# Kernel optimization log

Measured on AMD Instinct MI355X. Metric: run time of the kernel, lower is better.

## Reference

```python
import jax, jax.numpy as jnp
import numpy as np

NUM_HEADS = 16
D_MODEL = 1024
HEAD_DIM = D_MODEL // NUM_HEADS
EPS = 1e-6


def setup_inputs() -> dict:
    key = jax.random.key(0)
    ks = jax.random.split(key, 9)
    B, S, D = 4, 8192, D_MODEL
    scale = 1.0 / np.sqrt(D)  # variance_scaling(1.0, fan_in, normal) approx
    inputs_q = jax.random.normal(ks[0], (B, S, D), dtype=jnp.float32)
    Wq = jax.random.normal(ks[1], (D, D), dtype=jnp.float32) * scale
    Wk = jax.random.normal(ks[2], (D, D), dtype=jnp.float32) * scale
    Wv = jax.random.normal(ks[3], (D, D), dtype=jnp.float32) * scale
    Wo = jax.random.normal(ks[4], (D, D), dtype=jnp.float32) * scale
    bq = jnp.zeros((D,), jnp.float32)
    bk = jnp.zeros((D,), jnp.float32)
    bv = jnp.zeros((D,), jnp.float32)
    bo = jnp.zeros((D,), jnp.float32)
    return {"inputs_q": inputs_q, "Wq": Wq, "bq": bq, "Wk": Wk, "bk": bk,
            "Wv": Wv, "bv": bv, "Wo": Wo, "bo": bo}


def _feature_map(x):
    return jax.nn.elu(x) + 1.0


def reference(inputs_q, Wq, bq, Wk, bk, Wv, bv, Wo, bo):
    B, S, D = inputs_q.shape
    H, Dh = NUM_HEADS, HEAD_DIM
    # QKV projections (self-attention: k,v inputs default to q input)
    q = (inputs_q @ Wq + bq).reshape(B, S, H, Dh)
    k = (inputs_q @ Wk + bk).reshape(B, S, H, Dh)
    v = (inputs_q @ Wv + bv).reshape(B, S, H, Dh)
    q = _feature_map(q)
    k = _feature_map(k)
    # KV outer-product accumulation: [B, H, Dh, Dh]
    kv = jnp.einsum('bkhd,bkhm->bhdm', k, v)
    out = jnp.einsum('bqhd,bhdm->bqhm', q, kv)
    # normalizer: q . sum_k(k)
    normalizer = jnp.einsum('bqhd,bkhd->bqh', q, k)
    normalizer = jnp.maximum(normalizer, EPS)
    out = out / normalizer[..., None]
    out = out.reshape(B, S, D)
    return out @ Wo + bo
```

## Files before the change

### kernel.cpp

```cpp
#include <hip/hip_runtime.h>
#include <cstdint>
#include <cstddef>

#define D_MODEL 1024
#define SEQ 8192

typedef __bf16  bf16x8 __attribute__((ext_vector_type(8)));
typedef short   short8 __attribute__((ext_vector_type(8)));
typedef float   f32x4  __attribute__((ext_vector_type(4)));
typedef unsigned short ushort_t;

__device__ __forceinline__ ushort_t f2bf(float f) {
  uint32_t u = __builtin_bit_cast(uint32_t, f);
  u += 0x7FFFu + ((u >> 16) & 1u);
  return (ushort_t)(u >> 16);
}
__device__ __forceinline__ void gll16(const void* g, void* l) {
  __builtin_amdgcn_global_load_lds(
      (const __attribute__((address_space(1))) void*)g,
      (__attribute__((address_space(3))) void*)l, 16, 0, 0);
}
__device__ __forceinline__ void stage_half(const ushort_t* g, char* l0) {
  gll16(g, l0);
  gll16(g + 65536, l0 + 8192);
}

__global__ void k_convert_x(const float* __restrict__ x, ushort_t* __restrict__ xb, int n) {
  int i = (blockIdx.x * 256 + threadIdx.x) * 8;
  if (i >= n) return;
  float4 v0 = *(const float4*)(x + i);
  float4 v1 = *(const float4*)(x + i + 4);
  ushort_t o[8] = { f2bf(v0.x), f2bf(v0.y), f2bf(v0.z), f2bf(v0.w),
                    f2bf(v1.x), f2bf(v1.y), f2bf(v1.z), f2bf(v1.w) };
  *(short8*)(xb + i) = *(const short8*)o;
}

__global__ void k_transpose_w(const float* W0, const float* W1, const float* W2, const float* W3,
                              ushort_t* Tqkv, ushort_t* To) {
  const float* src; ushort_t* dst;
  switch (blockIdx.z) {
    case 0: src = W0; dst = Tqkv; break;
    case 1: src = W1; dst = Tqkv + (size_t)1024 * 1024; break;
    case 2: src = W2; dst = Tqkv + (size_t)2048 * 1024; break;
    default: src = W3; dst = To; break;
  }
  __shared__ float tile[64][65];
  int tx = threadIdx.x;
  int c = tx & 63, r0 = tx >> 6;
  int bx = blockIdx.x * 64, by = blockIdx.y * 64;
  #pragma unroll
  for (int i = 0; i < 16; i++) {
    int r = i * 4 + r0;
    tile[r][c] = src[(size_t)(by + r) * D_MODEL + bx + c];
  }
  __syncthreads();
  #pragma unroll
  for (int i = 0; i < 16; i++) {
    int r = i * 4 + r0;
    dst[(size_t)(bx + r) * D_MODEL + by + c] = f2bf(tile[c][r]);
  }
}

template<int MODE, int NY>
__global__ __launch_bounds__(512, 2) void k_gemm(const ushort_t* __restrict__ A,
                                                 const ushort_t* __restrict__ Bt,
                                                 const float* __restrict__ b0,
                                                 const float* __restrict__ b1,
                                                 const float* __restrict__ b2,
                                                 ushort_t* __restrict__ o0,
                                                 ushort_t* __restrict__ o1,
                                                 ushort_t* __restrict__ o2,
                                                 float* __restrict__ outf) {
  __shared__ __align__(16) char smem[131072];

  const int nwg = gridDim.x;
  const int bid0 = blockIdx.x;
  const int bid = (bid0 & 7) * (nwg >> 3) + (bid0 >> 3);
  const int xb = bid / NY, yb = bid % NY;
  const int m0 = xb * 256, n0 = yb * 256;

  const int tid = threadIdx.x;
  const int ln = tid & 63;
  const int w  = tid >> 6;
  const int wb = __builtin_amdgcn_readfirstlane(w);
  const int wm = wb >> 2, wn = wb & 3;

  const int srow = wb * 8 + (ln >> 3);
  const int schk = ((ln & 7) ^ ((ln >> 3) & 7)) * 8;
  const ushort_t* gA = A  + (size_t)(m0 + srow) * D_MODEL + schk;
  const ushort_t* gB = Bt + (size_t)(n0 + srow) * D_MODEL + schk;

#define STAGE_A(BUF, H, T) stage_half(gA + (size_t)(T) * 64 + (size_t)(H) * 131072, (BUF) + (H) * 16384 + wb * 1024)
#define STAGE_B(BUF, H, T) stage_half(gB + (size_t)(T) * 64 + (size_t)(H) * 131072, (BUF) + 32768 + (H) * 16384 + wb * 1024)

  char* cur = smem;
  char* nxt = smem + 65536;
  STAGE_B(cur, 0, 0); STAGE_B(cur, 1, 0); STAGE_A(cur, 0, 0); STAGE_A(cur, 1, 0);
  STAGE_B(nxt, 0, 1); STAGE_B(nxt, 1, 1); STAGE_A(nxt, 0, 1);
  asm volatile("s_waitcnt vmcnt(6)" ::: "memory");
  __builtin_amdgcn_s_barrier();

  f32x4 acc[8][4];
  #pragma unroll
  for (int i = 0; i < 8; i++)
    #pragma unroll
    for (int j = 0; j < 4; j++) acc[i][j] = (f32x4){0.f, 0.f, 0.f, 0.f};
  bf16x8 fa[4][2], fb0[2][2], fb1[2][2];

  const int ar  = ln & 15;
  const int cw0 = (((ln >> 4)    ) ^ (ln & 7)) << 4;
  const int cw1 = (((ln >> 4) + 4) ^ (ln & 7)) << 4;
  const int arow = wm * 128 + ar;
  const int brow = wn * 64 + ar;

#define LDA(MH) { _Pragma("unroll") for (int mi = 0; mi < 4; ++mi) { \
    const char* p_ = cur + ((arow + (MH) * 64 + mi * 16) << 7); \
    fa[mi][0] = *(const bf16x8*)(p_ + cw0); fa[mi][1] = *(const bf16x8*)(p_ + cw1); } }
#define LDB(FB, NH) { _Pragma("unroll") for (int nj = 0; nj < 2; ++nj) { \
    const char* p_ = cur + 32768 + ((brow + (NH) * 32 + nj * 16) << 7); \
    FB[nj][0] = *(const bf16x8*)(p_ + cw0); FB[nj][1] = *(const bf16x8*)(p_ + cw1); } }
#define QUAD(MH, NH, FB) { _Pragma("unroll") for (int mi = 0; mi < 4; ++mi) \
    _Pragma("unroll") for (int nj = 0; nj < 2; ++nj) { \
      acc[(MH)*4+mi][(NH)*2+nj] = __builtin_amdgcn_mfma_f32_16x16x32_bf16(fa[mi][0], FB[nj][0], acc[(MH)*4+mi][(NH)*2+nj], 0, 0, 0); \
      acc[(MH)*4+mi][(NH)*2+nj] = __builtin_amdgcn_mfma_f32_16x16x32_bf16(fa[mi][1], FB[nj][1], acc[(MH)*4+mi][(NH)*2+nj], 0, 0, 0); } }
#define PHASE_SYNC { __builtin_amdgcn_s_barrier(); \
                     asm volatile("s_waitcnt lgkmcnt(0)" ::: "memory"); \
                     __builtin_amdgcn_sched_barrier(0); }

  #pragma unroll 2
  for (int kt = 0; kt < 16; ++kt) {
    const bool st1 = (kt + 1 < 16);
    const bool st2 = (kt + 2 < 16);
    LDA(0); LDB(fb0, 0);
    if (st1) STAGE_A(nxt, 1, kt + 1);
    PHASE_SYNC;
    __builtin_amdgcn_s_setprio(1); QUAD(0, 0, fb0); __builtin_amdgcn_s_setprio(0);
    __builtin_amdgcn_s_barrier();
    LDB(fb1, 1);
    PHASE_SYNC;
    __builtin_amdgcn_s_setprio(1); QUAD(0, 1, fb1); __builtin_amdgcn_s_setprio(0);
    __builtin_amdgcn_s_barrier();
    LDA(1);
    if (st2) STAGE_B(cur, 0, kt + 2);
    PHASE_SYNC;
    __builtin_amdgcn_s_setprio(1); QUAD(1, 1, fb1); __builtin_amdgcn_s_setprio(0);
    __builtin_amdgcn_s_barrier();
    if (st2) { STAGE_B(cur, 1, kt + 2); STAGE_A(cur, 0, kt + 2); }
    __builtin_amdgcn_s_barrier();
    __builtin_amdgcn_s_setprio(1); QUAD(1, 0, fb0); __builtin_amdgcn_s_setprio(0);
    if (kt < 14)       asm volatile("s_waitcnt vmcnt(6)" ::: "memory");
    else if (kt == 14) asm volatile("s_waitcnt vmcnt(0)" ::: "memory");
    __builtin_amdgcn_s_barrier();
    char* t_ = cur; cur = nxt; nxt = t_;
  }
#undef STAGE_A
#undef STAGE_B
#undef LDA
#undef LDB
#undef QUAD
#undef PHASE_SYNC

  const int colb = ln & 15, rowb = (ln >> 4) * 4;

  if constexpr (MODE == 0) {
    const int region = yb >> 2;
    const int nl0 = (yb & 3) * 256;
    const float* bias = region == 0 ? b0 : (region == 1 ? b1 : b2);
    ushort_t* gout    = region == 0 ? o0 : (region == 1 ? o1 : o2);
    const bool act = region < 2;
    ushort_t* Cs = (ushort_t*)smem;
    #pragma unroll
    for (int j = 0; j < 4; ++j) {
      const int col = wn * 64 + j * 16 + colb;
      const float bv_ = bias[nl0 + col];
      #pragma unroll
      for (int i = 0; i < 8; ++i) {
        const int rb_ = wm * 128 + i * 16 + rowb;
        #pragma unroll
        for (int r = 0; r < 4; ++r) {
          float v = acc[i][j][r] + bv_;
          if (act) v = (v > 0.f) ? v + 1.f : __expf(v);
          const int row = rb_ + r;
          const int ch = col >> 3;
          Cs[row * 256 + ((ch ^ (row & 31)) << 3) + (col & 7)] = f2bf(v);
        }
      }
    }
    __syncthreads();
    #pragma unroll
    for (int c = 0; c < 16; ++c) {
      const int idx = c * 512 + tid;
      const int row = idx >> 5, ch = idx & 31;
      short8 t = *(const short8*)&Cs[row * 256 + ((ch ^ (row & 31)) << 3)];
      *(short8*)&gout[(size_t)(m0 + row) * D_MODEL + nl0 + ch * 8] = t;
    }
  } else {
    float* Cf = (float*)smem;
    #pragma unroll
    for (int h = 0; h < 2; ++h) {
      if (h) __syncthreads();
      if (wm == h) {
        #pragma unroll
        for (int j = 0; j < 4; ++j) {
          const int col = wn * 64 + j * 16 + colb;
          const float bv_ = b0[n0 + col];
          #pragma unroll
          for (int i = 0; i < 8; ++i) {
            const int rl = i * 16 + rowb;
            #pragma unroll
            for (int r = 0; r < 4; ++r) {
              const int row = rl + r;
              const int ch = col >> 2;
              Cf[row * 256 + ((ch ^ (row & 7)) << 2) + (col & 3)] = acc[i][j][r] + bv_;
            }
          }
        }
      }
      __syncthreads();
      #pragma unroll
      for (int c = 0; c < 16; ++c) {
        const int idx = c * 512 + tid;
        const int row = idx >> 6, ch = idx & 63;
        float4 t = *(const float4*)&Cf[row * 256 + ((ch ^ (row & 7)) << 2)];
        *(float4*)&outf[(size_t)(m0 + h * 128 + row) * D_MODEL + n0 + ch * 4] = t;
      }
    }
  }
}

__global__ __launch_bounds__(256) void k_kv_partial(const ushort_t* __restrict__ kmat,
                                                    const ushort_t* __restrict__ vmat,
                                                    float* __restrict__ part) {
  __shared__ __align__(16) ushort_t sbuf[4][2][2][512];
  const int tid = threadIdx.x, ln = tid & 63, w = tid >> 6;
  const int wb = __builtin_amdgcn_readfirstlane(w);
  const int bh = blockIdx.y, chunk = blockIdx.x;
  const int b = bh >> 4, h = bh & 15;
  const size_t cbase = ((size_t)b * SEQ + chunk * 1024 + w * 256) * D_MODEL + h * 64;
  const ushort_t* gk = kmat + cbase + (size_t)(ln >> 3) * D_MODEL + (ln & 7) * 8;
  const ushort_t* gv = vmat + cbase + (size_t)(ln >> 3) * D_MODEL + (ln & 7) * 8;

  float acc[8][8];
  float ksum[8];
  #pragma unroll
  for (int i = 0; i < 8; i++) { ksum[i] = 0.f;
    #pragma unroll
    for (int j = 0; j < 8; j++) acc[i][j] = 0.f; }

  const int r8 = (ln >> 3) * 8, c8 = (ln & 7) * 8;
  gll16(gk, &sbuf[wb][0][0][0]);
  gll16(gv, &sbuf[wb][0][1][0]);
  gk += 8 * D_MODEL; gv += 8 * D_MODEL;

  for (int bt = 0; bt < 32; bt++) {
    const int p = bt & 1;
    if (bt < 31) {
      gll16(gk, &sbuf[wb][p ^ 1][0][0]);
      gll16(gv, &sbuf[wb][p ^ 1][1][0]);
      gk += 8 * D_MODEL; gv += 8 * D_MODEL;
      __builtin_amdgcn_s_waitcnt(0x0F72);
    } else {
      __builtin_amdgcn_s_waitcnt(0x0F70);
    }
    #pragma unroll
    for (int s = 0; s < 8; s++) {
      short8 kk = *(const short8*)&sbuf[wb][p][0][s * 64 + r8];
      short8 vv = *(const short8*)&sbuf[wb][p][1][s * 64 + c8];
      float ka[8], va[8];
      #pragma unroll
      for (int i = 0; i < 8; i++) {
        ka[i] = __builtin_bit_cast(float, (uint32_t)(ushort_t)kk[i] << 16);
        va[i] = __builtin_bit_cast(float, (uint32_t)(ushort_t)vv[i] << 16);
      }
      #pragma unroll
      for (int i = 0; i < 8; i++) {
        ksum[i] += ka[i];
        #pragma unroll
        for (int j = 0; j < 8; j++) acc[i][j] += ka[i] * va[j];
      }
    }
  }
  float* p0 = part + ((size_t)bh * 32 + chunk * 4 + w) * 4160;
  #pragma unroll
  for (int i = 0; i < 8; i++)
    #pragma unroll
    for (int j = 0; j < 8; j++) p0[(r8 + i) * 64 + c8 + j] = acc[i][j];
  if ((ln & 7) == 0) {
    #pragma unroll
    for (int i = 0; i < 8; i++) p0[4096 + r8 + i] = ksum[i];
  }
}

__global__ void k_kv_reduce(const float* __restrict__ part, ushort_t* __restrict__ kvt) {
  const int bh = blockIdx.x, tid = threadIdx.x;
  const float* p0 = part + (size_t)bh * 32 * 4160;
  for (int idx = tid; idx < 4160; idx += 256) {
    float s = 0.f;
    #pragma unroll 4
    for (int c = 0; c < 32; c++) s += p0[(size_t)c * 4160 + idx];
    ushort_t bf = f2bf(s);
    if (idx < 4096) { int d = idx >> 6, m = idx & 63; kvt[(size_t)bh * 4160 + m * 64 + d] = bf; }
    else            { kvt[(size_t)bh * 4160 + 4096 + (idx - 4096)] = bf; }
  }
}

__global__ __launch_bounds__(256) void k_attn(const ushort_t* __restrict__ qmat,
                                              const ushort_t* __restrict__ kvt,
                                              ushort_t* __restrict__ attn) {
  __shared__ __align__(16) ushort_t kvs[65 * 80];
  __shared__ __align__(16) ushort_t qs[4][64 * 80];
  const int tid = threadIdx.x, ln = tid & 63, w = tid >> 6;
  const int bh = blockIdx.y, b = bh >> 4, h = bh & 15;

  for (int idx = tid; idx < 4160; idx += 256) {
    int m = idx >> 6, d = idx & 63;
    kvs[m * 80 + d] = kvt[(size_t)bh * 4160 + idx];
  }
  const size_t s0 = (size_t)b * SEQ + blockIdx.x * 256 + w * 64;
  #pragma unroll
  for (int c = 0; c < 8; c++) {
    int f = c * 64 + ln;
    int row = f >> 3, dg = (f & 7) * 8;
    short8 t = *(const short8*)&qmat[(s0 + row) * D_MODEL + h * 64 + dg];
    *(short8*)&qs[w][row * 80 + dg] = t;
  }
  __syncthreads();

  const int ar = ln & 15, aq = (ln >> 4) * 8;
  f32x4 acc[4][4], nacc[4];
  #pragma unroll
  for (int i = 0; i < 4; i++) { nacc[i] = (f32x4){0.f, 0.f, 0.f, 0.f};
    #pragma unroll
    for (int j = 0; j < 4; j++) acc[i][j] = (f32x4){0.f, 0.f, 0.f, 0.f}; }

  #pragma unroll
  for (int kk = 0; kk < 2; kk++) {
    const int ko = kk * 32 + aq;
    bf16x8 a[4], bb[4], bn;
    #pragma unroll
    for (int i = 0; i < 4; i++) a[i] = *(const bf16x8*)&qs[w][(i * 16 + ar) * 80 + ko];
    #pragma unroll
    for (int j = 0; j < 4; j++) bb[j] = *(const bf16x8*)&kvs[(j * 16 + ar) * 80 + ko];
    bn = *(const bf16x8*)&kvs[64 * 80 + ko];
    #pragma unroll
    for (int i = 0; i < 4; i++) {
      #pragma unroll
      for (int j = 0; j < 4; j++)
        acc[i][j] = __builtin_amdgcn_mfma_f32_16x16x32_bf16(a[i], bb[j], acc[i][j], 0, 0, 0);
      nacc[i] = __builtin_amdgcn_mfma_f32_16x16x32_bf16(a[i], bn, nacc[i], 0, 0, 0);
    }
  }

  const int colb = ln & 15, rowb = (ln >> 4) * 4;
  #pragma unroll
  for (int i = 0; i < 4; i++) {
    #pragma unroll
    for (int r = 0; r < 4; r++) {
      const int row = i * 16 + rowb + r;
      float nm = fmaxf(nacc[i][r], 1e-6f);
      float inv = 1.0f / nm;
      const size_t grow = s0 + row;
      #pragma unroll
      for (int j = 0; j < 4; j++) {
        float v = acc[i][j][r] * inv;
        attn[grow * D_MODEL + h * 64 + j * 16 + colb] = f2bf(v);
      }
    }
  }
}

extern "C" void kernel_launch(void* const* d_in, const int* in_sizes, int n_in,
                              void* d_out, int out_size, void* d_ws, size_t ws_size,
                              hipStream_t stream) {
  const float* x  = (const float*)d_in[0];
  const float* Wq = (const float*)d_in[1];
  const float* bq = (const float*)d_in[2];
  const float* Wk = (const float*)d_in[3];
  const float* bk = (const float*)d_in[4];
  const float* Wv = (const float*)d_in[5];
  const float* bv = (const float*)d_in[6];
  const float* Wo = (const float*)d_in[7];
  const float* bo = (const float*)d_in[8];
  float* out = (float*)d_out;

  const int M = in_sizes[0] / D_MODEL;
  const int B = M / SEQ;
  const int BH = B * 16;

  char* ws = (char*)d_ws;
  size_t off = 0;
  auto alloc = [&](size_t bytes) { char* p = ws + off; off += (bytes + 255) & ~(size_t)255; return p; };
  const size_t mb = (size_t)M * D_MODEL * 2;
  ushort_t* xb    = (ushort_t*)alloc(mb);
  ushort_t* qb    = (ushort_t*)alloc(mb);
  ushort_t* kb    = (ushort_t*)alloc(mb);
  ushort_t* vb    = (ushort_t*)alloc(mb);
  ushort_t* attnb = (ushort_t*)alloc(mb);
  ushort_t* wqkvt = (ushort_t*)alloc((size_t)3 * D_MODEL * D_MODEL * 2);
  ushort_t* wot   = (ushort_t*)alloc((size_t)D_MODEL * D_MODEL * 2);
  ushort_t* kvt   = (ushort_t*)alloc((size_t)BH * 4160 * 2);
  float*    part  = (float*)   alloc((size_t)BH * 32 * 4160 * 4);
  (void)ws_size; (void)n_in; (void)out_size;

  const int n = M * D_MODEL;
  k_convert_x<<<n / (256 * 8), 256, 0, stream>>>(x, xb, n);
  k_transpose_w<<<dim3(16, 16, 4), 256, 0, stream>>>(Wq, Wk, Wv, Wo, wqkvt, wot);

  k_gemm<0, 12><<<(M / 256) * 12, 512, 0, stream>>>(xb, wqkvt, bq, bk, bv, qb, kb, vb, nullptr);

  k_kv_partial<<<dim3(8, BH), 256, 0, stream>>>(kb, vb, part);
  k_kv_reduce<<<BH, 256, 0, stream>>>(part, kvt);
  k_attn<<<dim3(SEQ / 256, BH), 256, 0, stream>>>(qb, kvt, attnb);

  k_gemm<2, 4><<<(M / 256) * 4, 512, 0, stream>>>(attnb, wot, bo, nullptr, nullptr, nullptr, nullptr, nullptr, out);
}
```

Baseline: 673.6 us.

## Restructure GEMM main loop into four-phase pipeline with cross-tile fragment prefetch

Rewrites the 256x256 bf16 GEMM inner loop so each K-tile runs four phases over 32-row A slices, with all four B fragments held in registers. It prefetches the next tile's B fragments and first A slice from LDS while the current tile's MFMAs run. LDS waits drop from lgkmcnt(0) to finer lgkmcnt counts, and global-to-LDS staging is spread across the phases. The aim is to hide LDS and global latency behind MFMA work. The cost is more fragment registers and tight, hand-counted wait values that must exactly match the order of the asynchronous loads.

```diff
diff --git a/kernel.cpp b/kernel.cpp
--- a/kernel.cpp
+++ b/kernel.cpp
@@ -90,22 +90,21 @@
   const ushort_t* gA = A  + (size_t)(m0 + srow) * D_MODEL + schk;
   const ushort_t* gB = Bt + (size_t)(n0 + srow) * D_MODEL + schk;
 
-#define STAGE_A(BUF, H, T) stage_half(gA + (size_t)(T) * 64 + (size_t)(H) * 131072, (BUF) + (H) * 16384 + wb * 1024)
-#define STAGE_B(BUF, H, T) stage_half(gB + (size_t)(T) * 64 + (size_t)(H) * 131072, (BUF) + 32768 + (H) * 16384 + wb * 1024)
-
-  char* cur = smem;
-  char* nxt = smem + 65536;
-  STAGE_B(cur, 0, 0); STAGE_B(cur, 1, 0); STAGE_A(cur, 0, 0); STAGE_A(cur, 1, 0);
-  STAGE_B(nxt, 0, 1); STAGE_B(nxt, 1, 1); STAGE_A(nxt, 0, 1);
-  asm volatile("s_waitcnt vmcnt(6)" ::: "memory");
-  __builtin_amdgcn_s_barrier();
+#define STG_A(BASE, H, T) stage_half(gA + (size_t)(T) * 64 + (size_t)(H) * 131072, smem + (BASE) + (H) * 16384 + wb * 1024)
+#define STG_B(BASE, H, T) stage_half(gB + (size_t)(T) * 64 + (size_t)(H) * 131072, smem + (BASE) + 32768 + (H) * 16384 + wb * 1024)
+
+#define VMW_(N) asm volatile("s_waitcnt vmcnt(" #N ")" ::: "memory")
+#define VMW(N)  VMW_(N)
+#define LGW_(N) asm volatile("s_waitcnt lgkmcnt(" #N ")" ::: "memory")
+#define LGW(N)  do { LGW_(N); __builtin_amdgcn_sched_barrier(0); } while (0)
 
   f32x4 acc[8][4];
   #pragma unroll
   for (int i = 0; i < 8; i++)
     #pragma unroll
     for (int j = 0; j < 4; j++) acc[i][j] = (f32x4){0.f, 0.f, 0.f, 0.f};
-  bf16x8 fa[4][2], fb0[2][2], fb1[2][2];
+  bf16x8 aX[2][2], aY[2][2];
+  bf16x8 bX[4][2], bY[4][2];
 
   const int ar  = ln & 15;
   const int cw0 = (((ln >> 4)    ) ^ (ln & 7)) << 4;
@@ -113,52 +112,77 @@
   const int arow = wm * 128 + ar;
   const int brow = wn * 64 + ar;
 
-#define LDA(MH) { _Pragma("unroll") for (int mi = 0; mi < 4; ++mi) { \
-    const char* p_ = cur + ((arow + (MH) * 64 + mi * 16) << 7); \
-    fa[mi][0] = *(const bf16x8*)(p_ + cw0); fa[mi][1] = *(const bf16x8*)(p_ + cw1); } }
-#define LDB(FB, NH) { _Pragma("unroll") for (int nj = 0; nj < 2; ++nj) { \
-    const char* p_ = cur + 32768 + ((brow + (NH) * 32 + nj * 16) << 7); \
-    FB[nj][0] = *(const bf16x8*)(p_ + cw0); FB[nj][1] = *(const bf16x8*)(p_ + cw1); } }
-#define QUAD(MH, NH, FB) { _Pragma("unroll") for (int mi = 0; mi < 4; ++mi) \
-    _Pragma("unroll") for (int nj = 0; nj < 2; ++nj) { \
-      acc[(MH)*4+mi][(NH)*2+nj] = __builtin_amdgcn_mfma_f32_16x16x32_bf16(fa[mi][0], FB[nj][0], acc[(MH)*4+mi][(NH)*2+nj], 0, 0, 0); \
-      acc[(MH)*4+mi][(NH)*2+nj] = __builtin_amdgcn_mfma_f32_16x16x32_bf16(fa[mi][1], FB[nj][1], acc[(MH)*4+mi][(NH)*2+nj], 0, 0, 0); } }
-#define PHASE_SYNC { __builtin_amdgcn_s_barrier(); \
-                     asm volatile("s_waitcnt lgkmcnt(0)" ::: "memory"); \
-                     __builtin_amdgcn_sched_barrier(0); }
-
-  #pragma unroll 2
-  for (int kt = 0; kt < 16; ++kt) {
-    const bool st1 = (kt + 1 < 16);
-    const bool st2 = (kt + 2 < 16);
-    LDA(0); LDB(fb0, 0);
-    if (st1) STAGE_A(nxt, 1, kt + 1);
-    PHASE_SYNC;
-    __builtin_amdgcn_s_setprio(1); QUAD(0, 0, fb0); __builtin_amdgcn_s_setprio(0);
-    __builtin_amdgcn_s_barrier();
-    LDB(fb1, 1);
-    PHASE_SYNC;
-    __builtin_amdgcn_s_setprio(1); QUAD(0, 1, fb1); __builtin_amdgcn_s_setprio(0);
-    __builtin_amdgcn_s_barrier();
-    LDA(1);
-    if (st2) STAGE_B(cur, 0, kt + 2);
-    PHASE_SYNC;
-    __builtin_amdgcn_s_setprio(1); QUAD(1, 1, fb1); __builtin_amdgcn_s_setprio(0);
-    __builtin_amdgcn_s_barrier();
-    if (st2) { STAGE_B(cur, 1, kt + 2); STAGE_A(cur, 0, kt + 2); }
-    __builtin_amdgcn_s_barrier();
-    __builtin_amdgcn_s_setprio(1); QUAD(1, 0, fb0); __builtin_amdgcn_s_setprio(0);
-    if (kt < 14)       asm volatile("s_waitcnt vmcnt(6)" ::: "memory");
-    else if (kt == 14) asm volatile("s_waitcnt vmcnt(0)" ::: "memory");
-    __builtin_amdgcn_s_barrier();
-    char* t_ = cur; cur = nxt; nxt = t_;
-  }
-#undef STAGE_A
-#undef STAGE_B
-#undef LDA
-#undef LDB
-#undef QUAD
-#undef PHASE_SYNC
+#define LDA2(DST, BASE, CH) { _Pragma("unroll") for (int m_ = 0; m_ < 2; ++m_) { \
+    const char* p_ = smem + (BASE) + ((arow + (CH) * 32 + m_ * 16) << 7); \
+    DST[m_][0] = *(const bf16x8*)(p_ + cw0); DST[m_][1] = *(const bf16x8*)(p_ + cw1); } }
+#define LDB2(DST, BASE, J0) { _Pragma("unroll") for (int j_ = 0; j_ < 2; ++j_) { \
+    const char* p_ = smem + (BASE) + 32768 + ((brow + ((J0) + j_) * 16) << 7); \
+    DST[(J0) + j_][0] = *(const bf16x8*)(p_ + cw0); DST[(J0) + j_][1] = *(const bf16x8*)(p_ + cw1); } }
+#define MF8(P, ASET, BSET) { _Pragma("unroll") for (int m_ = 0; m_ < 2; ++m_) \
+    _Pragma("unroll") for (int j_ = 0; j_ < 4; ++j_) { \
+      acc[(P)*2+m_][j_] = __builtin_amdgcn_mfma_f32_16x16x32_bf16(ASET[m_][0], BSET[j_][0], acc[(P)*2+m_][j_], 0, 0, 0); \
+      acc[(P)*2+m_][j_] = __builtin_amdgcn_mfma_f32_16x16x32_bf16(ASET[m_][1], BSET[j_][1], acc[(P)*2+m_][j_], 0, 0, 0); } }
+
+#define ENDBAR { __builtin_amdgcn_s_barrier(); __builtin_amdgcn_sched_barrier(0); }
+
+#define TILE(T, CUR, NXT, BC, BN, H1, H2, L1, L2, L3, V2) { \
+     \
+    LDA2(aY, CUR, 1); \
+    if (H1) STG_A(NXT, 0, (T) + 1); \
+    __builtin_amdgcn_s_barrier(); \
+    LGW(4); \
+    __builtin_amdgcn_s_setprio(1); MF8(0, aX, BC); __builtin_amdgcn_s_setprio(0); \
+    VMW(2); \
+    ENDBAR; \
+     \
+    LDA2(aX, CUR, 2); \
+    if (H1) LDB2(BN, NXT, 0); \
+    if (H1) STG_A(NXT, 1, (T) + 1); \
+    __builtin_amdgcn_s_barrier(); \
+    LGW(L1); \
+    __builtin_amdgcn_s_setprio(1); MF8(1, aY, BC); __builtin_amdgcn_s_setprio(0); \
+    ENDBAR; \
+     \
+    LDA2(aY, CUR, 3); \
+    if (H1) LDB2(BN, NXT, 2); \
+    if (H2) STG_B(CUR, 0, (T) + 2); \
+    __builtin_amdgcn_s_barrier(); \
+    LGW(L2); \
+    __builtin_amdgcn_s_setprio(1); MF8(2, aX, BC); __builtin_amdgcn_s_setprio(0); \
+    VMW(V2); \
+    ENDBAR; \
+     \
+    if (H1) LDA2(aX, NXT, 0); \
+    if (H2) STG_B(CUR, 1, (T) + 2); \
+    __builtin_amdgcn_s_barrier(); \
+    LGW(L3); \
+    __builtin_amdgcn_s_setprio(1); MF8(3, aY, BC); __builtin_amdgcn_s_setprio(0); \
+    ENDBAR; \
+  }
+
+  STG_A(0, 0, 0); STG_A(0, 1, 0); STG_B(0, 0, 0); STG_B(0, 1, 0);
+  STG_B(65536, 0, 1); STG_B(65536, 1, 1);
+  VMW(4);
+  __builtin_amdgcn_s_barrier();
+  __builtin_amdgcn_sched_barrier(0);
+  LDA2(aX, 0, 0);
+  LDB2(bX, 0, 0); LDB2(bX, 0, 2);
+
+  #pragma unroll 1
+  for (int kt = 0; kt < 14; kt += 2) {
+    TILE(kt,     0,     65536, bX, bY, true, true, 8, 8, 4, 2);
+    TILE(kt + 1, 65536, 0,     bY, bX, true, true, 8, 8, 4, 2);
+  }
+  TILE(14, 0,     65536, bX, bY, true,  false, 8, 8, 4, 0);
+  TILE(15, 65536, 0,     bY, bX, false, false, 4, 4, 0, 2);
+
+#undef STG_A
+#undef STG_B
+#undef LDA2
+#undef LDB2
+#undef MF8
+#undef TILE
+#undef ENDBAR
 
   const int colb = ln & 15, rowb = (ln >> 4) * 4;
 
@@ -226,6 +250,10 @@
       }
     }
   }
+#undef VMW_
+#undef VMW
+#undef LGW_
+#undef LGW
 }
 
 __global__ __launch_bounds__(256) void k_kv_partial(const ushort_t* __restrict__ kmat,
```

Result: no change. 668.5 us (-0.8%).
